# Performance work log

Measured on AMD Instinct MI355X. Metric: run time of the kernel, lower is better.

The kernel has to match this reference:

```python
import jax, jax.numpy as jnp
import numpy as np

B, N, C_IN, C_OUT, CHEB_K, EMBED = 64, 2048, 64, 64, 3, 16


def setup_inputs() -> dict:
    key = jax.random.key(0)
    k1, k2, k3, k4 = jax.random.split(key, 4)
    return {
        "graph": 0,  # unused placeholder, matches original signature
        "node_feature": jax.random.normal(k1, (B, N, C_IN), dtype=jnp.float32),
        "node_embeddings": jax.random.normal(k2, (N, EMBED), dtype=jnp.float32),
        "weights_pool": jax.random.normal(k3, (EMBED, CHEB_K, C_IN, C_OUT), dtype=jnp.float32),
        "bias_pool": jax.random.normal(k4, (EMBED, C_OUT), dtype=jnp.float32),
    }


def reference(graph, node_feature, node_embeddings, weights_pool, bias_pool):
    x = node_feature                      # [B, N, C]
    n = node_embeddings.shape[0]
    # adaptive adjacency: softmax(relu(E E^T)) row-wise
    supports = jax.nn.softmax(jax.nn.relu(node_embeddings @ node_embeddings.T), axis=1)  # [N, N]
    # Chebyshev polynomial basis
    support_set = [jnp.eye(n, dtype=supports.dtype), supports]
    for _ in range(2, CHEB_K):
        support_set.append(2.0 * supports @ support_set[-1] - support_set[-2])
    supports_k = jnp.stack(support_set, axis=0)  # [K, N, N]
    # per-node dynamic weights / bias
    weights = jnp.einsum('nd,dkio->nkio', node_embeddings, weights_pool)  # [N, K, I, O]
    bias = node_embeddings @ bias_pool                                    # [N, O]
    # graph aggregation over Chebyshev orders
    x_g = jnp.einsum('knm,bmc->bnkc', supports_k, x)                      # [B, N, K, C]
    # per-node weighted contraction
    out = jnp.einsum('bnki,nkio->bno', x_g, weights) + bias               # [B, N, O]
    return out
```

## Files before the change

kernel.cpp:

```cpp
#include <hip/hip_runtime.h>
#include <hip/hip_bf16.h>

#define BB 64
#define NN 2048
#define CC 64
#define DD 16

typedef __attribute__((ext_vector_type(8))) short bf16x8;
typedef __attribute__((ext_vector_type(4))) float f32x4;

__device__ __forceinline__ ushort f2bf(float f) {
  unsigned u = __float_as_uint(f);
  u += 0x7fffu + ((u >> 16) & 1u);
  return (ushort)(u >> 16);
}
__device__ __forceinline__ float b2f(ushort h) {
  return __uint_as_float(((unsigned)h) << 16);
}

#define GLOAD16(g, l)                                                 \
  __builtin_amdgcn_global_load_lds(                                   \
      (const __attribute__((address_space(1))) void*)(g),             \
      (__attribute__((address_space(3))) void*)(l), 16, 0, 0)

__global__ __launch_bounds__(256) void transpose_x_kernel(
    const float* __restrict__ X, ushort* __restrict__ Xt,
    ushort* __restrict__ Xnb) {
  const int b = blockIdx.y;
  const int m0 = blockIdx.x * 256;
  const int t = threadIdx.x;
  __shared__ ushort xs[256 * 64];

#pragma unroll
  for (int it = 0; it < 16; ++it) {
    const int idx = it * 256 + t;
    const int m = idx >> 4;
    const int cq = (idx & 15) * 4;
    float4 v = *(const float4*)&X[(size_t)b * NN * CC + (size_t)(m0 + m) * CC + cq];
    ushort4 h;
    h.x = f2bf(v.x); h.y = f2bf(v.y); h.z = f2bf(v.z); h.w = f2bf(v.w);
    *(ushort4*)((char*)xs + m * 128 + ((cq * 2) ^ ((m & 7) << 4))) = h;
    if (Xnb)
      *(ushort4*)&Xnb[((size_t)(m0 + m) * BB + b) * CC + cq] = h;
  }
  __syncthreads();

  const int c = t >> 2;
  const int mb = (t & 3) * 64;
#pragma unroll
  for (int s = 0; s < 8; ++s) {
    unsigned w0 = 0, w1 = 0, w2 = 0, w3 = 0;
#pragma unroll
    for (int j = 0; j < 8; ++j) {
      const int m = mb + s * 8 + j;
      const ushort hv =
          *(const ushort*)((const char*)xs + m * 128 + ((2 * c) ^ ((m & 7) << 4)));
      const unsigned uv = (unsigned)hv << ((j & 1) * 16);
      if (j < 2) w0 |= uv; else if (j < 4) w1 |= uv;
      else if (j < 6) w2 |= uv; else w3 |= uv;
    }
    uint4 pk = {w0, w1, w2, w3};
    *(uint4*)&Xt[(size_t)b * CC * NN + (size_t)c * NN + m0 + mb + s * 8] = pk;
  }
}

__global__ __launch_bounds__(256) void wpt_kernel(
    const float* __restrict__ Wp, ushort* __restrict__ Wpt) {
  const int g = blockIdx.x * 256 + threadIdx.x;
  const int d = g / 1536;
  const int rem = g % 1536;
  const int o = rem / 24;
  const int ki0 = (rem % 24) * 8;
  bf16x8 h;
#pragma unroll
  for (int j = 0; j < 8; ++j)
    h[j] = (short)f2bf(Wp[d * 12288 + (ki0 + j) * 64 + o]);
  *(bf16x8*)&Wpt[d * 12288 + o * 192 + ki0] = h;
}

__global__ __launch_bounds__(256) void supports_kernel(
    const float* __restrict__ E, ushort* __restrict__ S) {
  const int n = blockIdx.x;
  const int t = threadIdx.x;

  __shared__ float en[DD];
  if (t < DD) en[t] = E[n * DD + t];
  __syncthreads();

  float e[DD];
#pragma unroll
  for (int d = 0; d < DD; ++d) e[d] = en[d];

  float vals[8];
  float vmax = 0.f;
#pragma unroll
  for (int j = 0; j < 8; ++j) {
    const int m = j * 256 + t;
    const float4* Em = (const float4*)&E[m * DD];
    float4 v0 = Em[0], v1 = Em[1], v2 = Em[2], v3 = Em[3];
    float dot = e[0]*v0.x + e[1]*v0.y + e[2]*v0.z + e[3]*v0.w
              + e[4]*v1.x + e[5]*v1.y + e[6]*v1.z + e[7]*v1.w
              + e[8]*v2.x + e[9]*v2.y + e[10]*v2.z + e[11]*v2.w
              + e[12]*v3.x + e[13]*v3.y + e[14]*v3.z + e[15]*v3.w;
    dot = fmaxf(dot, 0.f);
    vals[j] = dot;
    vmax = fmaxf(vmax, dot);
  }

  __shared__ float red[256];
  red[t] = vmax;
  __syncthreads();
  for (int s = 128; s > 0; s >>= 1) {
    if (t < s) red[t] = fmaxf(red[t], red[t + s]);
    __syncthreads();
  }
  vmax = red[0];
  __syncthreads();

  float sum = 0.f;
#pragma unroll
  for (int j = 0; j < 8; ++j) {
    vals[j] = __expf(vals[j] - vmax);
    sum += vals[j];
  }
  red[t] = sum;
  __syncthreads();
  for (int s = 128; s > 0; s >>= 1) {
    if (t < s) red[t] += red[t + s];
    __syncthreads();
  }
  const float inv = 1.f / red[0];

#pragma unroll
  for (int j = 0; j < 8; ++j)
    S[(size_t)n * NN + j * 256 + t] = f2bf(vals[j] * inv);
}

__global__ __launch_bounds__(256) void spmm_t_kernel(
    const ushort* __restrict__ At, const ushort* __restrict__ S,
    ushort* __restrict__ Yt, ushort* __restrict__ Yn, int nb) {
  const int b  = blockIdx.x;
  const int n0 = blockIdx.y * 256;
  const int t  = threadIdx.x;
  const int w  = t >> 6;
  const int l  = t & 63;

  __shared__ ushort Als[2][64 * 64];
  __shared__ ushort Bls[2][256 * 64];

  const char* Abase = (const char*)(At + (size_t)b * CC * NN);
  const char* Sbase = (const char*)S + (size_t)n0 * (NN * 2);

  f32x4 acc[4][4];
#pragma unroll
  for (int i = 0; i < 4; ++i)
#pragma unroll
    for (int j = 0; j < 4; ++j) acc[i][j] = (f32x4)0.f;

  const int lkb = (l & 7) * 16;
  const int lrw = w * 8 + (l >> 3);

  auto stage = [&](int buf, int mt) {
#pragma unroll
    for (int q = 0; q < 2; ++q) {
      const int row = q * 32 + lrw;
      GLOAD16(Abase + (size_t)row * (NN * 2) + mt * 2 + (lkb ^ ((row & 7) << 4)),
              (char*)Als[buf] + q * 4096 + w * 1024);
    }
#pragma unroll
    for (int q = 0; q < 8; ++q) {
      const int row = q * 32 + lrw;
      GLOAD16(Sbase + (size_t)row * (NN * 2) + mt * 2 + (lkb ^ ((row & 7) << 4)),
              (char*)Bls[buf] + q * 4096 + w * 1024);
    }
  };

  stage(0, 0);
  int cur = 0;
  for (int it = 0; it < 32; ++it) {
    const int nmt = ((it + 1) & 31) * 64;
    stage(cur ^ 1, nmt);
    asm volatile("s_waitcnt vmcnt(10)" ::: "memory");
    __builtin_amdgcn_s_barrier();
    __builtin_amdgcn_sched_barrier(0);

#pragma unroll
    for (int kk = 0; kk < 2; ++kk) {
      const int kb = kk * 64 + (l >> 4) * 16;
      bf16x8 a[4], bv[4];
#pragma unroll
      for (int cf = 0; cf < 4; ++cf) {
        const int c = cf * 16 + (l & 15);
        a[cf] = *(const bf16x8*)((const char*)Als[cur] + c * 128 +
                                 (kb ^ ((c & 7) << 4)));
      }
#pragma unroll
      for (int nf = 0; nf < 4; ++nf) {
        const int r = w * 64 + nf * 16 + (l & 15);
        bv[nf] = *(const bf16x8*)((const char*)Bls[cur] + r * 128 +
                                  (kb ^ ((r & 7) << 4)));
      }
#pragma unroll
      for (int cf = 0; cf < 4; ++cf)
#pragma unroll
        for (int nf = 0; nf < 4; ++nf)
          acc[cf][nf] = __builtin_amdgcn_mfma_f32_16x16x32_bf16(
              a[cf], bv[nf], acc[cf][nf], 0, 0, 0);
    }

    __builtin_amdgcn_sched_barrier(0);
    __builtin_amdgcn_s_barrier();
    cur ^= 1;
  }

  const int nw = n0 + w * 64;
#pragma unroll
  for (int cf = 0; cf < 4; ++cf) {
#pragma unroll
    for (int nf = 0; nf < 4; ++nf) {
      const int n = nw + nf * 16 + (l & 15);
      const int cb = cf * 16 + (l >> 4) * 4;
      ushort h0 = f2bf(acc[cf][nf][0]);
      ushort h1 = f2bf(acc[cf][nf][1]);
      ushort h2 = f2bf(acc[cf][nf][2]);
      ushort h3 = f2bf(acc[cf][nf][3]);
      if (Yt) {
        ushort* p = Yt + (size_t)b * CC * NN + (size_t)cb * NN + n;
        p[0] = h0; p[NN] = h1; p[2 * NN] = h2; p[3 * NN] = h3;
      }
      if (Yn) {
        ushort4 pk = {h0, h1, h2, h3};
        if (nb)
          *(ushort4*)(Yn + ((size_t)n * BB + b) * CC + cb) = pk;
        else
          *(ushort4*)(Yn + ((size_t)b * NN + n) * CC + cb) = pk;
      }
    }
  }
}

__global__ __launch_bounds__(512) void out_kernel_direct(
    const float* __restrict__ E, const ushort* __restrict__ Wpt,
    const float* __restrict__ Bp, const ushort* __restrict__ Xnb,
    const ushort* __restrict__ Y1nb, const ushort* __restrict__ Y2nb,
    float* __restrict__ Out) {
  const int n0 = blockIdx.x * 2;
  const int t = threadIdx.x;

  __shared__ ushort Wt[2][64 * 192];
  __shared__ float bsh[2][64];
  __shared__ float esh[2][DD];

  if (t < 2 * DD) esh[t >> 4][t & 15] = E[(n0 + (t >> 4)) * DD + (t & 15)];
  __syncthreads();
  float ea[DD], eb[DD];
#pragma unroll
  for (int d = 0; d < DD; ++d) { ea[d] = esh[0][d]; eb[d] = esh[1][d]; }

  if (t < 128) {
    const int node = t >> 6, o = t & 63;
    const float* e = node ? eb : ea;
    float bsum = 0.f;
#pragma unroll
    for (int d = 0; d < DD; ++d) bsum = fmaf(e[d], Bp[d * 64 + o], bsum);
    bsh[node][o] = bsum;
  }

#pragma unroll
  for (int it = 0; it < 3; ++it) {
    const int boff = it * 8192 + t * 16;
    float acc0[8] = {}, acc1[8] = {};
#pragma unroll
    for (int d = 0; d < DD; ++d) {
      bf16x8 wv = *(const bf16x8*)((const char*)Wpt + d * 24576 + boff);
#pragma unroll
      for (int u = 0; u < 8; ++u) {
        const float f = b2f((ushort)wv[u]);
        acc0[u] = fmaf(ea[d], f, acc0[u]);
        acc1[u] = fmaf(eb[d], f, acc1[u]);
      }
    }
    bf16x8 h0, h1;
#pragma unroll
    for (int u = 0; u < 8; ++u) {
      h0[u] = (short)f2bf(acc0[u]);
      h1[u] = (short)f2bf(acc1[u]);
    }
    const int o = boff / 384;
    const int sw = (boff % 384) ^ ((o & 7) << 4);
    *(bf16x8*)((char*)Wt[0] + o * 384 + sw) = h0;
    *(bf16x8*)((char*)Wt[1] + o * 384 + sw) = h1;
  }
  __syncthreads();

  const int w8 = t >> 6, l = t & 63;
  const int node = w8 >> 2, q = w8 & 3;
  const int br = (q & 1) * 32, oc = (q >> 1) * 32;
  const int n = n0 + node;
  const char* wtn = (const char*)Wt[node];
  const ushort* xsrc  = Xnb  + (size_t)n * BB * CC;
  const ushort* y1src = Y1nb + (size_t)n * BB * CC;
  const ushort* y2src = Y2nb + (size_t)n * BB * CC;
  const int kq = (l >> 4) * 8;

  f32x4 acc[2][2];
#pragma unroll
  for (int i = 0; i < 2; ++i)
#pragma unroll
    for (int j = 0; j < 2; ++j) acc[i][j] = (f32x4)0.f;

#pragma unroll
  for (int s = 0; s < 6; ++s) {
    const int kk = s >> 1;
    const int ich = (s & 1) * 32 + kq;
    bf16x8 av[2];
#pragma unroll
    for (int i = 0; i < 2; ++i) {
      const int b = br + i * 16 + (l & 15);
      const int off = b * CC + ich;
      if (kk == 0) {
        av[i] = *(const bf16x8*)&xsrc[off];
      } else if (kk == 1) {
        av[i] = *(const bf16x8*)&y1src[off];
      } else {
        bf16x8 y2 = *(const bf16x8*)&y2src[off];
        bf16x8 xv = *(const bf16x8*)&xsrc[off];
        bf16x8 hv;
#pragma unroll
        for (int u = 0; u < 8; ++u)
          hv[u] = (short)f2bf(2.f * b2f((ushort)y2[u]) - b2f((ushort)xv[u]));
        av[i] = hv;
      }
    }
    bf16x8 bv[2];
    const int kb = s * 64 + (l >> 4) * 16;
#pragma unroll
    for (int j = 0; j < 2; ++j) {
      const int row = oc + j * 16 + (l & 15);
      bv[j] = *(const bf16x8*)(wtn + row * 384 + (kb ^ ((row & 7) << 4)));
    }
#pragma unroll
    for (int i = 0; i < 2; ++i)
#pragma unroll
      for (int j = 0; j < 2; ++j)
        acc[i][j] = __builtin_amdgcn_mfma_f32_16x16x32_bf16(av[i], bv[j],
                                                            acc[i][j], 0, 0, 0);
  }

  const size_t NC = (size_t)NN * CC;
#pragma unroll
  for (int i = 0; i < 2; ++i) {
#pragma unroll
    for (int j = 0; j < 2; ++j) {
      const int o = oc + j * 16 + (l & 15);
      const int bb = br + i * 16 + (l >> 4) * 4;
      const float bo = bsh[node][o];
#pragma unroll
      for (int r = 0; r < 4; ++r)
        Out[(size_t)(bb + r) * NC + (size_t)n * CC + o] = acc[i][j][r] + bo;
    }
  }
}

__global__ __launch_bounds__(512) void out_kernel(
    const float* __restrict__ E, const ushort* __restrict__ Wpt,
    const float* __restrict__ Bp, const float* __restrict__ X,
    const ushort* __restrict__ Y1n, const ushort* __restrict__ Y1t,
    const ushort* __restrict__ Y2n, float* __restrict__ Out) {
  const int n0 = blockIdx.x * 2;
  const int t = threadIdx.x;

  __shared__ ushort Wt[2][64 * 192];
  __shared__ ushort xg[2][64 * 192];
  __shared__ float bsh[2][64];
  __shared__ float esh[2][DD];

  if (t < 2 * DD) esh[t >> 4][t & 15] = E[(n0 + (t >> 4)) * DD + (t & 15)];
  __syncthreads();
  float ea[DD], eb[DD];
#pragma unroll
  for (int d = 0; d < DD; ++d) { ea[d] = esh[0][d]; eb[d] = esh[1][d]; }

  if (t < 128) {
    const int node = t >> 6, o = t & 63;
    const float* e = node ? eb : ea;
    float bsum = 0.f;
#pragma unroll
    for (int d = 0; d < DD; ++d) bsum = fmaf(e[d], Bp[d * 64 + o], bsum);
    bsh[node][o] = bsum;
  }

#pragma unroll
  for (int it = 0; it < 3; ++it) {
    const int boff = it * 8192 + t * 16;
    float acc0[8] = {}, acc1[8] = {};
#pragma unroll
    for (int d = 0; d < DD; ++d) {
      bf16x8 wv = *(const bf16x8*)((const char*)Wpt + d * 24576 + boff);
#pragma unroll
      for (int u = 0; u < 8; ++u) {
        const float f = b2f((ushort)wv[u]);
        acc0[u] = fmaf(ea[d], f, acc0[u]);
        acc1[u] = fmaf(eb[d], f, acc1[u]);
      }
    }
    bf16x8 h0, h1;
#pragma unroll
    for (int u = 0; u < 8; ++u) {
      h0[u] = (short)f2bf(acc0[u]);
      h1[u] = (short)f2bf(acc1[u]);
    }
    const int o = boff / 384;
    const int sw = (boff % 384) ^ ((o & 7) << 4);
    *(bf16x8*)((char*)Wt[0] + o * 384 + sw) = h0;
    *(bf16x8*)((char*)Wt[1] + o * 384 + sw) = h1;
  }

  {
    const int node = t >> 8, tt = t & 255;
    const int b = tt >> 2, i0 = (tt & 3) * 16;
    const int n = n0 + node;
    const size_t NC = (size_t)NN * CC;
    const size_t gbase = (size_t)b * NC + (size_t)n * CC + i0;
    char* xgn = (char*)xg[node];
    float xv[16];
#pragma unroll
    for (int j = 0; j < 4; ++j) {
      float4 v = *(const float4*)&X[gbase + j * 4];
      xv[j * 4 + 0] = v.x; xv[j * 4 + 1] = v.y;
      xv[j * 4 + 2] = v.z; xv[j * 4 + 3] = v.w;
    }
#pragma unroll
    for (int h = 0; h < 2; ++h) {
      bf16x8 hv;
#pragma unroll
      for (int u = 0; u < 8; ++u) hv[u] = (short)f2bf(xv[h * 8 + u]);
      const int ki = i0 + h * 8;
      *(bf16x8*)(xgn + b * 384 + ((ki * 2) ^ ((b & 7) << 4))) = hv;
    }
    if (Y1n) {
#pragma unroll
      for (int h = 0; h < 2; ++h) {
        bf16x8 hv = *(const bf16x8*)&Y1n[gbase + h * 8];
        const int ki = 64 + i0 + h * 8;
        *(bf16x8*)(xgn + b * 384 + ((ki * 2) ^ ((b & 7) << 4))) = hv;
      }
    } else {
#pragma unroll
      for (int h = 0; h < 2; ++h) {
        bf16x8 hv;
#pragma unroll
        for (int u = 0; u < 8; ++u)
          hv[u] = (short)Y1t[(size_t)b * NC + (size_t)(i0 + h * 8 + u) * NN + n];
        const int ki = 64 + i0 + h * 8;
        *(bf16x8*)(xgn + b * 384 + ((ki * 2) ^ ((b & 7) << 4))) = hv;
      }
    }
#pragma unroll
    for (int h = 0; h < 2; ++h) {
      bf16x8 y2 = *(const bf16x8*)&Y2n[gbase + h * 8];
      bf16x8 hv;
#pragma unroll
      for (int u = 0; u < 8; ++u)
        hv[u] = (short)f2bf(2.f * b2f((ushort)y2[u]) - xv[h * 8 + u]);
      const int ki = 128 + i0 + h * 8;
      *(bf16x8*)(xgn + b * 384 + ((ki * 2) ^ ((b & 7) << 4))) = hv;
    }
  }
  __syncthreads();

  const int w8 = t >> 6, l = t & 63;
  const int node = w8 >> 2, q = w8 & 3;
  const int br = (q & 1) * 32, oc = (q >> 1) * 32;
  const char* xgn = (const char*)xg[node];
  const char* wtn = (const char*)Wt[node];

  f32x4 acc[2][2];
#pragma unroll
  for (int i = 0; i < 2; ++i)
#pragma unroll
    for (int j = 0; j < 2; ++j) acc[i][j] = (f32x4)0.f;

#pragma unroll
  for (int s = 0; s < 6; ++s) {
    const int kb = s * 64 + (l >> 4) * 16;
    bf16x8 av[2], bv[2];
#pragma unroll
    for (int i = 0; i < 2; ++i) {
      const int row = br + i * 16 + (l & 15);
      av[i] = *(const bf16x8*)(xgn + row * 384 + (kb ^ ((row & 7) << 4)));
    }
#pragma unroll
    for (int j = 0; j < 2; ++j) {
      const int row = oc + j * 16 + (l & 15);
      bv[j] = *(const bf16x8*)(wtn + row * 384 + (kb ^ ((row & 7) << 4)));
    }
#pragma unroll
    for (int i = 0; i < 2; ++i)
#pragma unroll
      for (int j = 0; j < 2; ++j)
        acc[i][j] = __builtin_amdgcn_mfma_f32_16x16x32_bf16(av[i], bv[j],
                                                            acc[i][j], 0, 0, 0);
  }

  const size_t NC = (size_t)NN * CC;
  const int n = n0 + node;
#pragma unroll
  for (int i = 0; i < 2; ++i) {
#pragma unroll
    for (int j = 0; j < 2; ++j) {
      const int o = oc + j * 16 + (l & 15);
      const int bb = br + i * 16 + (l >> 4) * 4;
      const float bo = bsh[node][o];
#pragma unroll
      for (int r = 0; r < 4; ++r)
        Out[(size_t)(bb + r) * NC + (size_t)n * CC + o] = acc[i][j][r] + bo;
    }
  }
}

extern "C" void kernel_launch(void* const* d_in, const int* in_sizes, int n_in,
                              void* d_out, int out_size, void* d_ws, size_t ws_size,
                              hipStream_t stream) {
  const float* x  = (const float*)d_in[1];
  const float* E  = (const float*)d_in[2];
  const float* Wp = (const float*)d_in[3];
  const float* Bp = (const float*)d_in[4];
  float* out = (float*)d_out;

  const size_t szS  = (size_t)NN * NN * 2;
  const size_t szY  = (size_t)BB * NN * CC * 2;
  const size_t szWp = (size_t)DD * 3 * CC * CC * 2;
  ushort* Sb  = (ushort*)d_ws;
  ushort* Xt  = (ushort*)((char*)d_ws + szS);
  ushort* Wpt = (ushort*)((char*)d_ws + szS + szY);
  char*   P   = (char*)d_ws + szS + szY + szWp;
  ushort* Y1t = (ushort*)d_out;
  ushort* Y2  = Xt;

  const bool direct = ws_size >= szS + 3 * szY + szWp;

  ushort* Xnb  = direct ? (ushort*)P : nullptr;
  ushort* Y1nb = direct ? (ushort*)(P + szY) : nullptr;
  ushort* Y1n  = direct ? nullptr : (ushort*)P;

  transpose_x_kernel<<<dim3(NN / 256, BB), 256, 0, stream>>>(x, Xt, Xnb);
  wpt_kernel<<<96, 256, 0, stream>>>(Wp, Wpt);
  supports_kernel<<<NN, 256, 0, stream>>>(E, Sb);

  dim3 g2(BB, NN / 256);
  spmm_t_kernel<<<g2, 256, 0, stream>>>(Xt, Sb, Y1t,
                                        direct ? Y1nb : Y1n, direct ? 1 : 0);
  spmm_t_kernel<<<g2, 256, 0, stream>>>(Y1t, Sb, nullptr, Y2, direct ? 1 : 0);

  if (direct)
    out_kernel_direct<<<NN / 2, 512, 0, stream>>>(E, Wpt, Bp, Xnb, Y1nb, Y2,
                                                  out);
  else
    out_kernel<<<NN / 2, 512, 0, stream>>>(E, Wpt, Bp, x, Y1n, Y1t, Y2, out);
}
```

Measured before the change: 180.5 us.

## Drop node-major staging copies and gather per-batch rows in out kernel via LDS

```diff
diff --git a/kernel.cpp b/kernel.cpp
--- a/kernel.cpp
+++ b/kernel.cpp
@@ -24,8 +24,7 @@
       (__attribute__((address_space(3))) void*)(l), 16, 0, 0)
 
 __global__ __launch_bounds__(256) void transpose_x_kernel(
-    const float* __restrict__ X, ushort* __restrict__ Xt,
-    ushort* __restrict__ Xnb) {
+    const float* __restrict__ X, ushort* __restrict__ Xt) {
   const int b = blockIdx.y;
   const int m0 = blockIdx.x * 256;
   const int t = threadIdx.x;
@@ -40,8 +39,6 @@
     ushort4 h;
     h.x = f2bf(v.x); h.y = f2bf(v.y); h.z = f2bf(v.z); h.w = f2bf(v.w);
     *(ushort4*)((char*)xs + m * 128 + ((cq * 2) ^ ((m & 7) << 4))) = h;
-    if (Xnb)
-      *(ushort4*)&Xnb[((size_t)(m0 + m) * BB + b) * CC + cq] = h;
   }
   __syncthreads();
 
@@ -138,7 +135,7 @@
 
 __global__ __launch_bounds__(256) void spmm_t_kernel(
     const ushort* __restrict__ At, const ushort* __restrict__ S,
-    ushort* __restrict__ Yt, ushort* __restrict__ Yn, int nb) {
+    ushort* __restrict__ Yt, ushort* __restrict__ Yn) {
   const int b  = blockIdx.x;
   const int n0 = blockIdx.y * 256;
   const int t  = threadIdx.x;
@@ -230,24 +227,22 @@
       }
       if (Yn) {
         ushort4 pk = {h0, h1, h2, h3};
-        if (nb)
-          *(ushort4*)(Yn + ((size_t)n * BB + b) * CC + cb) = pk;
-        else
-          *(ushort4*)(Yn + ((size_t)b * NN + n) * CC + cb) = pk;
-      }
-    }
-  }
-}
-
-__global__ __launch_bounds__(512) void out_kernel_direct(
+        *(ushort4*)(Yn + (size_t)b * NN * CC + (size_t)n * CC + cb) = pk;
+      }
+    }
+  }
+}
+
+__global__ __launch_bounds__(512) void out_kernel_c(
     const float* __restrict__ E, const ushort* __restrict__ Wpt,
-    const float* __restrict__ Bp, const ushort* __restrict__ Xnb,
-    const ushort* __restrict__ Y1nb, const ushort* __restrict__ Y2nb,
+    const float* __restrict__ Bp, const float* __restrict__ X,
+    const ushort* __restrict__ Y1n, const ushort* __restrict__ Y2n,
     float* __restrict__ Out) {
   const int n0 = blockIdx.x * 2;
   const int t = threadIdx.x;
 
   __shared__ ushort Wt[2][64 * 192];
+  __shared__ ushort xg[2][16 * 192];
   __shared__ float bsh[2][64];
   __shared__ float esh[2][DD];
 
@@ -291,74 +286,87 @@
     *(bf16x8*)((char*)Wt[0] + o * 384 + sw) = h0;
     *(bf16x8*)((char*)Wt[1] + o * 384 + sw) = h1;
   }
-  __syncthreads();
 
   const int w8 = t >> 6, l = t & 63;
   const int node = w8 >> 2, q = w8 & 3;
-  const int br = (q & 1) * 32, oc = (q >> 1) * 32;
-  const int n = n0 + node;
+  const int oc = q * 16;
   const char* wtn = (const char*)Wt[node];
-  const ushort* xsrc  = Xnb  + (size_t)n * BB * CC;
-  const ushort* y1src = Y1nb + (size_t)n * BB * CC;
-  const ushort* y2src = Y2nb + (size_t)n * BB * CC;
-  const int kq = (l >> 4) * 8;
-
-  f32x4 acc[2][2];
-#pragma unroll
-  for (int i = 0; i < 2; ++i)
-#pragma unroll
-    for (int j = 0; j < 2; ++j) acc[i][j] = (f32x4)0.f;
-
-#pragma unroll
-  for (int s = 0; s < 6; ++s) {
-    const int kk = s >> 1;
-    const int ich = (s & 1) * 32 + kq;
-    bf16x8 av[2];
-#pragma unroll
-    for (int i = 0; i < 2; ++i) {
-      const int b = br + i * 16 + (l & 15);
-      const int off = b * CC + ich;
-      if (kk == 0) {
-        av[i] = *(const bf16x8*)&xsrc[off];
-      } else if (kk == 1) {
-        av[i] = *(const bf16x8*)&y1src[off];
+  const size_t NC = (size_t)NN * CC;
+
+  const int snode = t >> 8, tt = t & 255;
+  const int sb = tt >> 4;
+  const int part = tt & 15;
+  const int ki0 = part * 16;
+  const int sn = n0 + snode;
+  char* xgw = (char*)xg[snode];
+
+  for (int chunk = 0; chunk < 4; ++chunk) {
+    __syncthreads();
+    if (part < 12) {
+      const int gb = chunk * 16 + sb;
+      const size_t gbase = (size_t)gb * NC + (size_t)sn * CC;
+      const int swz = (sb & 7) << 4;
+      if (ki0 < 64) {
+        float xv[16];
+#pragma unroll
+        for (int j = 0; j < 4; ++j) {
+          float4 v = *(const float4*)&X[gbase + ki0 + j * 4];
+          xv[j*4+0] = v.x; xv[j*4+1] = v.y; xv[j*4+2] = v.z; xv[j*4+3] = v.w;
+        }
+#pragma unroll
+        for (int h = 0; h < 2; ++h) {
+          bf16x8 hv;
+#pragma unroll
+          for (int u = 0; u < 8; ++u) hv[u] = (short)f2bf(xv[h * 8 + u]);
+          *(bf16x8*)(xgw + sb * 384 + (((ki0 + h * 8) * 2) ^ swz)) = hv;
+        }
+      } else if (ki0 < 128) {
+        const int i0 = ki0 - 64;
+#pragma unroll
+        for (int h = 0; h < 2; ++h) {
+          bf16x8 hv = *(const bf16x8*)&Y1n[gbase + i0 + h * 8];
+          *(bf16x8*)(xgw + sb * 384 + (((ki0 + h * 8) * 2) ^ swz)) = hv;
+        }
       } else {
-        bf16x8 y2 = *(const bf16x8*)&y2src[off];
-        bf16x8 xv = *(const bf16x8*)&xsrc[off];
-        bf16x8 hv;
-#pragma unroll
-        for (int u = 0; u < 8; ++u)
-          hv[u] = (short)f2bf(2.f * b2f((ushort)y2[u]) - b2f((ushort)xv[u]));
-        av[i] = hv;
-      }
-    }
-    bf16x8 bv[2];
-    const int kb = s * 64 + (l >> 4) * 16;
-#pragma unroll
-    for (int j = 0; j < 2; ++j) {
-      const int row = oc + j * 16 + (l & 15);
-      bv[j] = *(const bf16x8*)(wtn + row * 384 + (kb ^ ((row & 7) << 4)));
-    }
-#pragma unroll
-    for (int i = 0; i < 2; ++i)
-#pragma unroll
-      for (int j = 0; j < 2; ++j)
-        acc[i][j] = __builtin_amdgcn_mfma_f32_16x16x32_bf16(av[i], bv[j],
-                                                            acc[i][j], 0, 0, 0);
-  }
-
-  const size_t NC = (size_t)NN * CC;
-#pragma unroll
-  for (int i = 0; i < 2; ++i) {
-#pragma unroll
-    for (int j = 0; j < 2; ++j) {
-      const int o = oc + j * 16 + (l & 15);
-      const int bb = br + i * 16 + (l >> 4) * 4;
-      const float bo = bsh[node][o];
-#pragma unroll
-      for (int r = 0; r < 4; ++r)
-        Out[(size_t)(bb + r) * NC + (size_t)n * CC + o] = acc[i][j][r] + bo;
-    }
+        const int i0 = ki0 - 128;
+        float xv[16];
+#pragma unroll
+        for (int j = 0; j < 4; ++j) {
+          float4 v = *(const float4*)&X[gbase + i0 + j * 4];
+          xv[j*4+0] = v.x; xv[j*4+1] = v.y; xv[j*4+2] = v.z; xv[j*4+3] = v.w;
+        }
+#pragma unroll
+        for (int h = 0; h < 2; ++h) {
+          bf16x8 y2 = *(const bf16x8*)&Y2n[gbase + i0 + h * 8];
+          bf16x8 hv;
+#pragma unroll
+          for (int u = 0; u < 8; ++u)
+            hv[u] = (short)f2bf(2.f * b2f((ushort)y2[u]) - xv[h * 8 + u]);
+          *(bf16x8*)(xgw + sb * 384 + (((ki0 + h * 8) * 2) ^ swz)) = hv;
+        }
+      }
+    }
+    __syncthreads();
+
+    const char* xgn = (const char*)xg[node];
+    f32x4 acc = (f32x4)0.f;
+#pragma unroll
+    for (int s = 0; s < 6; ++s) {
+      const int kb = s * 64 + (l >> 4) * 16;
+      const int rb = l & 15;
+      bf16x8 av = *(const bf16x8*)(xgn + rb * 384 + (kb ^ ((rb & 7) << 4)));
+      const int ro = oc + (l & 15);
+      bf16x8 bv = *(const bf16x8*)(wtn + ro * 384 + (kb ^ ((ro & 7) << 4)));
+      acc = __builtin_amdgcn_mfma_f32_16x16x32_bf16(av, bv, acc, 0, 0, 0);
+    }
+
+    const int o = oc + (l & 15);
+    const float bo = bsh[node][o];
+    const int bb = chunk * 16 + (l >> 4) * 4;
+    const size_t obase = (size_t)(n0 + node) * CC + o;
+#pragma unroll
+    for (int r = 0; r < 4; ++r)
+      Out[(size_t)(bb + r) * NC + obase] = acc[r] + bo;
   }
 }
 
@@ -533,29 +541,23 @@
   const size_t szWp = (size_t)DD * 3 * CC * CC * 2;
   ushort* Sb  = (ushort*)d_ws;
   ushort* Xt  = (ushort*)((char*)d_ws + szS);
-  ushort* Wpt = (ushort*)((char*)d_ws + szS + szY);
-  char*   P   = (char*)d_ws + szS + szY + szWp;
-  ushort* Y1t = (ushort*)d_out;
-  ushort* Y2  = Xt;
-
-  const bool direct = ws_size >= szS + 3 * szY + szWp;
-
-  ushort* Xnb  = direct ? (ushort*)P : nullptr;
-  ushort* Y1nb = direct ? (ushort*)(P + szY) : nullptr;
-  ushort* Y1n  = direct ? nullptr : (ushort*)P;
-
-  transpose_x_kernel<<<dim3(NN / 256, BB), 256, 0, stream>>>(x, Xt, Xnb);
+  ushort* Y1t = (ushort*)((char*)d_ws + szS + szY);
+  ushort* Wpt = (ushort*)((char*)d_ws + szS + 2 * szY);
+  ushort* Y1n = (ushort*)((char*)d_ws + szS + 2 * szY + szWp);
+  ushort* Y2n = Xt;
+  const bool haveY1n = ws_size >= szS + 3 * szY + szWp;
+
+  transpose_x_kernel<<<dim3(NN / 256, BB), 256, 0, stream>>>(x, Xt);
   wpt_kernel<<<96, 256, 0, stream>>>(Wp, Wpt);
   supports_kernel<<<NN, 256, 0, stream>>>(E, Sb);
 
   dim3 g2(BB, NN / 256);
-  spmm_t_kernel<<<g2, 256, 0, stream>>>(Xt, Sb, Y1t,
-                                        direct ? Y1nb : Y1n, direct ? 1 : 0);
-  spmm_t_kernel<<<g2, 256, 0, stream>>>(Y1t, Sb, nullptr, Y2, direct ? 1 : 0);
-
-  if (direct)
-    out_kernel_direct<<<NN / 2, 512, 0, stream>>>(E, Wpt, Bp, Xnb, Y1nb, Y2,
-                                                  out);
+  spmm_t_kernel<<<g2, 256, 0, stream>>>(Xt, Sb, Y1t, haveY1n ? Y1n : nullptr);
+  spmm_t_kernel<<<g2, 256, 0, stream>>>(Y1t, Sb, nullptr, Y2n);
+
+  if (haveY1n)
+    out_kernel_c<<<NN / 2, 512, 0, stream>>>(E, Wpt, Bp, x, Y1n, Y2n, out);
   else
-    out_kernel<<<NN / 2, 512, 0, stream>>>(E, Wpt, Bp, x, Y1n, Y1t, Y2, out);
-}
+    out_kernel<<<NN / 2, 512, 0, stream>>>(E, Wpt, Bp, x, nullptr, Y1t, Y2n,
+                                           out);
+}
```

New measurement: 188.2 us. +4.3%, slower.
